# Performance work log

Measured on AMD Instinct MI355X. Metric: run time of the kernel, lower is better.

Reference implementation:

```python
import jax, jax.numpy as jnp
import numpy as np

B, S, D, H, R = 4, 4096, 1024, 16, 256
DEPTH = D // H  # 64
FILTER_H = 3


def setup_inputs() -> dict:
    key = jax.random.key(0)
    ks = jax.random.split(key, 10)
    s = 0.02
    return {
        "x": jax.random.normal(ks[0], (B, S, D), jnp.float32),
        "wq": jax.random.normal(ks[1], (D, D), jnp.float32) * s,
        "wk": jax.random.normal(ks[2], (D, D), jnp.float32) * s,
        "wv": jax.random.normal(ks[3], (D, D), jnp.float32) * s,
        "E": jax.random.normal(ks[4], (H, S, R), jnp.float32) * s,
        "F": jax.random.normal(ks[5], (H, S, R), jnp.float32) * s,
        "conv_kernel": jax.random.normal(ks[6], (FILTER_H, R, 1, 1), jnp.float32) * s,  # HWIO
        "conv_bias": jnp.zeros((1,), jnp.float32),
        "wo": jax.random.normal(ks[7], (D, D), jnp.float32) * s,
        "bo": jnp.zeros((D,), jnp.float32),
    }


def _split_heads(t):
    # [B,S,D] -> [B,H,S,depth]
    return t.reshape(B, S, H, DEPTH).transpose(0, 2, 1, 3)


def reference(x, wq, wk, wv, E, F, conv_kernel, conv_bias, wo, bo):
    q = _split_heads(x @ wq)
    k = _split_heads(x @ wk)
    v = _split_heads(x @ wv)
    # low-rank projections along sequence: [B,H,R,depth]
    k_proj = jnp.einsum('bhnd,hnr->bhrd', k, E)
    v_proj = jnp.einsum('bhnd,hnr->bhrd', v, F)
    scale = 1.0 / jnp.sqrt(jnp.asarray(DEPTH, jnp.float32))
    scores = jnp.einsum('bhsd,bhrd->bhsr', q, k_proj) * scale  # [B,H,S,R]
    # Conv2D(filters=1, kernel=(3,R), padding='same') over [B*H, S, R, 1]
    xi = scores.reshape(B * H, S, R, 1)
    conv = jax.lax.conv_general_dilated(
        xi, conv_kernel, window_strides=(1, 1), padding='SAME',
        dimension_numbers=('NHWC', 'HWIO', 'NHWC'))
    scores = (conv + conv_bias).reshape(B, H, S, R)
    attn = jax.nn.softmax(scores, axis=-1)
    out = jnp.einsum('bhsr,bhrd->bhsd', attn, v_proj)
    out = out.transpose(0, 2, 1, 3).reshape(B, S, D)
    return out @ wo + bo
```

## Files before the change

### kernel.cpp

```cpp
#include <hip/hip_runtime.h>

#define B_ 4
#define S_ 4096
#define D_ 1024
#define H_ 16
#define R_ 256
#define DP_ 64

typedef short bf16x8 __attribute__((ext_vector_type(8)));
typedef short short4v __attribute__((ext_vector_type(4)));
typedef float f32x4 __attribute__((ext_vector_type(4)));

__device__ __forceinline__ short f2bf(float f) {
  unsigned u = __builtin_bit_cast(unsigned, f);
  u += 0x7fffu + ((u >> 16) & 1u);
  return (short)(u >> 16);
}
__device__ __forceinline__ float bf2f(short s) {
  unsigned u = ((unsigned)(unsigned short)s) << 16;
  return __builtin_bit_cast(float, u);
}

__global__ __launch_bounds__(256) void convert_x_kernel(const float* __restrict__ x,
                                                        short* __restrict__ xb) {
  const int n8 = (B_ * S_ * D_) / 8;
  int i = blockIdx.x * 256 + threadIdx.x;
  const int stride = gridDim.x * 256;
  for (; i < n8; i += stride) {
    const float4 a = ((const float4*)x)[2 * i];
    const float4 b = ((const float4*)x)[2 * i + 1];
    bf16x8 o;
    o[0] = f2bf(a.x); o[1] = f2bf(a.y); o[2] = f2bf(a.z); o[3] = f2bf(a.w);
    o[4] = f2bf(b.x); o[5] = f2bf(b.y); o[6] = f2bf(b.z); o[7] = f2bf(b.w);
    ((bf16x8*)xb)[i] = o;
  }
}

__global__ __launch_bounds__(256) void transpose_w_kernel(
    const float* __restrict__ w0, const float* __restrict__ w1,
    const float* __restrict__ w2, const float* __restrict__ w3,
    short* __restrict__ wT) {
  __shared__ float tile[64][65];
  const int z = blockIdx.z;
  const float* W = (z == 0) ? w0 : (z == 1) ? w1 : (z == 2) ? w2 : w3;
  short* out = wT + (size_t)z * (D_ * D_);
  const int k0 = blockIdx.y * 64;
  const int n0 = blockIdx.x * 64;
  const int tid = threadIdx.x;
#pragma unroll
  for (int q = 0; q < 4; ++q) {
    const int rr = (tid >> 4) + (q << 4);
    const float4 v = *(const float4*)&W[(size_t)(k0 + rr) * D_ + n0 + ((tid & 15) << 2)];
    tile[rr][(tid & 15) * 4 + 0] = v.x;
    tile[rr][(tid & 15) * 4 + 1] = v.y;
    tile[rr][(tid & 15) * 4 + 2] = v.z;
    tile[rr][(tid & 15) * 4 + 3] = v.w;
  }
  __syncthreads();
#pragma unroll
  for (int q = 0; q < 2; ++q) {
    const int nr = (tid >> 3) + (q << 5);
    const int c8 = (tid & 7) << 3;
    bf16x8 o;
#pragma unroll
    for (int j = 0; j < 8; ++j) o[j] = f2bf(tile[c8 + j][nr]);
    *(bf16x8*)&out[(size_t)(n0 + nr) * D_ + k0 + c8] = o;
  }
}

__global__ __launch_bounds__(256) void build_T_kernel(const float* __restrict__ ck,
                                                      short* __restrict__ Tt) {
  const int idx = blockIdx.x * 256 + threadIdx.x;
  const int i = idx >> 16;
  const int r = (idx >> 8) & 255;
  const int c = idx & 255;
  const int j = c - r + 127;
  const float v = (j >= 0 && j < 256) ? ck[i * 256 + j] * 0.125f : 0.f;
  Tt[idx] = f2bf(v);
}

template <bool OUT_BF16>
__device__ __forceinline__ void mfma_gemm_1024(const short* __restrict__ A,
                                               const short* __restrict__ Bt,
                                               void* __restrict__ Cout,
                                               const float* __restrict__ bias) {
  __shared__ short As[128 * 32];
  __shared__ short Bs[128 * 32];
  const int tid = threadIdx.x;
  const int w = tid >> 6, l = tid & 63;
  const int m0 = blockIdx.y * 128, n0 = blockIdx.x * 128;

  const int srow = (w << 5) + (l >> 2);
  const int gchunk = l & 3;
  const int schunkX = ((gchunk ^ (srow & 3)) << 4);
  const short* Ag = A + (size_t)(m0 + srow) * D_ + (gchunk << 3);
  const short* Bg = Bt + (size_t)(n0 + srow) * D_ + (gchunk << 3);
  char* AsW = (char*)As + srow * 64 + schunkX;
  char* BsW = (char*)Bs + srow * 64 + schunkX;

  const int wr = ((w >> 1) << 6);
  const int wc = ((w & 1) << 6);
  const int fx = (l >> 4) ^ (l & 3);

  f32x4 acc[4][4];
#pragma unroll
  for (int i = 0; i < 4; ++i)
#pragma unroll
    for (int j = 0; j < 4; ++j) acc[i][j] = (f32x4){0.f, 0.f, 0.f, 0.f};

  for (int k0 = 0; k0 < D_; k0 += 32) {
    const bf16x8 a0 = *(const bf16x8*)(Ag + k0);
    const bf16x8 a1 = *(const bf16x8*)(Ag + (size_t)16 * D_ + k0);
    const bf16x8 b0 = *(const bf16x8*)(Bg + k0);
    const bf16x8 b1 = *(const bf16x8*)(Bg + (size_t)16 * D_ + k0);
    __syncthreads();
    *(bf16x8*)AsW = a0;
    *(bf16x8*)(AsW + 1024) = a1;
    *(bf16x8*)BsW = b0;
    *(bf16x8*)(BsW + 1024) = b1;
    __syncthreads();
    bf16x8 af[4], bfv[4];
#pragma unroll
    for (int t = 0; t < 4; ++t) {
      const int ar = wr + (t << 4) + (l & 15);
      af[t] = *(const bf16x8*)((char*)As + ar * 64 + (fx << 4));
      const int br = wc + (t << 4) + (l & 15);
      bfv[t] = *(const bf16x8*)((char*)Bs + br * 64 + (fx << 4));
    }
#pragma unroll
    for (int i = 0; i < 4; ++i)
#pragma unroll
      for (int j = 0; j < 4; ++j)
        acc[i][j] = __builtin_amdgcn_mfma_f32_16x16x32_bf16(af[i], bfv[j], acc[i][j], 0, 0, 0);
  }

#pragma unroll
  for (int i = 0; i < 4; ++i) {
#pragma unroll
    for (int r = 0; r < 4; ++r) {
      const int row = m0 + wr + (i << 4) + ((l >> 4) << 2) + r;
#pragma unroll
      for (int j = 0; j < 4; ++j) {
        const int col = n0 + wc + (j << 4) + (l & 15);
        const float vv = acc[i][j][r];
        if (OUT_BF16)
          ((short*)Cout)[(size_t)row * D_ + col] = f2bf(vv);
        else
          ((float*)Cout)[(size_t)row * D_ + col] = vv + bias[col];
      }
    }
  }
}

__global__ __launch_bounds__(256) void qkv_mfma_kernel(
    const short* __restrict__ xb, const short* __restrict__ wT,
    short* __restrict__ qb, short* __restrict__ kb, short* __restrict__ vb) {
  const int z = blockIdx.z;
  const short* Bt = wT + (size_t)z * (D_ * D_);
  short* C = (z == 0) ? qb : (z == 1) ? kb : vb;
  mfma_gemm_1024<true>(xb, Bt, C, nullptr);
}

__global__ __launch_bounds__(256) void out_mfma_kernel(
    const short* __restrict__ aob, const short* __restrict__ woT,
    const float* __restrict__ bo, float* __restrict__ out) {
  mfma_gemm_1024<false>(aob, woT, out, bo);
}

__global__ __launch_bounds__(256) void transpose_kv_kernel(
    const short* __restrict__ kb, const short* __restrict__ vb,
    short* __restrict__ kTb, short* __restrict__ vTb) {
  __shared__ short tile[64 * 80];
  const int tid = threadIdx.x;
  const int n0 = blockIdx.x * 64;
  const int bh = blockIdx.y;
  const int b = bh >> 4, h = bh & 15;
  const short* src = blockIdx.z ? vb : kb;
  short* dst = blockIdx.z ? vTb : kTb;
#pragma unroll
  for (int q = 0; q < 2; ++q) {
    const int idx = tid + q * 256;
    const int n = idx >> 3, c = idx & 7;
    *(bf16x8*)&tile[n * 80 + c * 8] =
        *(const bf16x8*)&src[((size_t)b * S_ + n0 + n) * D_ + h * DP_ + c * 8];
  }
  __syncthreads();
#pragma unroll
  for (int q = 0; q < 2; ++q) {
    const int idx = tid + q * 256;
    const int d = idx >> 3, cc = idx & 7;
    bf16x8 o;
#pragma unroll
    for (int j = 0; j < 8; ++j) o[j] = tile[(cc * 8 + j) * 80 + d];
    *(bf16x8*)&dst[((size_t)bh * DP_ + d) * S_ + n0 + cc * 8] = o;
  }
}

__global__ __launch_bounds__(256) void transpose_EF_kernel(
    const float* __restrict__ E, const float* __restrict__ F,
    short* __restrict__ ETb, short* __restrict__ FTb) {
  __shared__ float tile[64][65];
  const int tid = threadIdx.x;
  const int n0 = blockIdx.x * 64;
  const int r0 = blockIdx.y * 64;
  const int hz = blockIdx.z;
  const int h = hz & 15;
  const float* src = (hz < 16) ? E : F;
  short* dst = (hz < 16) ? ETb : FTb;
  const float* base = src + ((size_t)h * S_ + n0) * R_ + r0;
#pragma unroll
  for (int q = 0; q < 4; ++q) {
    const int n = (tid >> 4) + q * 16;
    const int r4 = (tid & 15) << 2;
    const float4 v = *(const float4*)&base[(size_t)n * R_ + r4];
    tile[n][r4 + 0] = v.x; tile[n][r4 + 1] = v.y;
    tile[n][r4 + 2] = v.z; tile[n][r4 + 3] = v.w;
  }
  __syncthreads();
#pragma unroll
  for (int q = 0; q < 2; ++q) {
    const int r = (tid >> 3) + q * 32;
    const int n8 = (tid & 7) << 3;
    bf16x8 o;
#pragma unroll
    for (int j = 0; j < 8; ++j) o[j] = f2bf(tile[n8 + j][r]);
    *(bf16x8*)&dst[((size_t)h * R_ + r0 + r) * S_ + n0 + n8] = o;
  }
}

__global__ __launch_bounds__(256) void proj_mfma_kernel(
    const short* __restrict__ ETb, const short* __restrict__ FTb,
    const short* __restrict__ kTb, const short* __restrict__ vTb,
    short* __restrict__ kprojTb, short* __restrict__ vprojTb) {
  __shared__ short As[128 * 64];
  __shared__ short Bs[64 * 64];
  const int tid = threadIdx.x;
  const int w = tid >> 6, l = tid & 63;
  const int l15 = l & 15, l16 = l >> 4;
  const int r0 = blockIdx.x * 128;
  const int bh = blockIdx.y;
  const int h = bh & 15;
  const int z = blockIdx.z;
  const short* Ab = (z ? FTb : ETb) + ((size_t)h * R_ + r0) * S_;
  const short* Bb = (z ? vTb : kTb) + (size_t)bh * DP_ * S_;
  short* outp = z ? vprojTb : kprojTb;
  const int wm = w >> 1, wn = w & 1;

  f32x4 acc[4][2];
#pragma unroll
  for (int mt = 0; mt < 4; ++mt)
#pragma unroll
    for (int nt = 0; nt < 2; ++nt) acc[mt][nt] = (f32x4){0.f, 0.f, 0.f, 0.f};

  for (int k0 = 0; k0 < S_; k0 += 64) {
    bf16x8 a[4], bq[2];
#pragma unroll
    for (int j = 0; j < 4; ++j) {
      const int idx = tid + j * 256;
      const int ar = idx >> 3, c = idx & 7;
      a[j] = *(const bf16x8*)&Ab[(size_t)ar * S_ + k0 + c * 8];
    }
#pragma unroll
    for (int j = 0; j < 2; ++j) {
      const int idx = tid + j * 256;
      const int br = idx >> 3, c = idx & 7;
      bq[j] = *(const bf16x8*)&Bb[(size_t)br * S_ + k0 + c * 8];
    }
    __syncthreads();
#pragma unroll
    for (int j = 0; j < 4; ++j) {
      const int idx = tid + j * 256;
      const int ar = idx >> 3, c = idx & 7;
      *(bf16x8*)((char*)As + ar * 128 + ((c ^ (ar & 7)) << 4)) = a[j];
    }
#pragma unroll
    for (int j = 0; j < 2; ++j) {
      const int idx = tid + j * 256;
      const int br = idx >> 3, c = idx & 7;
      *(bf16x8*)((char*)Bs + br * 128 + ((c ^ (br & 7)) << 4)) = bq[j];
    }
    __syncthreads();
#pragma unroll
    for (int kk = 0; kk < 2; ++kk) {
      bf16x8 af[4], bfr[2];
#pragma unroll
      for (int mt = 0; mt < 4; ++mt) {
        const int row = wm * 64 + mt * 16 + l15;
        af[mt] = *(const bf16x8*)((char*)As + row * 128 + (((kk * 4 + l16) ^ (row & 7)) << 4));
      }
#pragma unroll
      for (int nt = 0; nt < 2; ++nt) {
        const int row = wn * 32 + nt * 16 + l15;
        bfr[nt] = *(const bf16x8*)((char*)Bs + row * 128 + (((kk * 4 + l16) ^ (row & 7)) << 4));
      }
#pragma unroll
      for (int mt = 0; mt < 4; ++mt)
#pragma unroll
        for (int nt = 0; nt < 2; ++nt)
          acc[mt][nt] = __builtin_amdgcn_mfma_f32_16x16x32_bf16(af[mt], bfr[nt], acc[mt][nt], 0, 0, 0);
    }
  }

#pragma unroll
  for (int mt = 0; mt < 4; ++mt)
#pragma unroll
    for (int nt = 0; nt < 2; ++nt) {
      const int d = wn * 32 + nt * 16 + l15;
      const int rbase = r0 + wm * 64 + mt * 16 + l16 * 4;
      short4v o;
#pragma unroll
      for (int rr = 0; rr < 4; ++rr) o[rr] = f2bf(acc[mt][nt][rr]);
      *(short4v*)&outp[((size_t)bh * DP_ + d) * R_ + rbase] = o;
    }
}

__global__ __launch_bounds__(256) void build_M_kernel(
    const short* __restrict__ Tt, const short* __restrict__ kprojTb,
    short* __restrict__ Mb) {
  const int tid = threadIdx.x;
  const int w = tid >> 6, l = tid & 63;
  const int l15 = l & 15, l16 = l >> 4;
  const int r0 = blockIdx.x * 64 + w * 16;
  const int bh = blockIdx.y;
  const short* Kp = kprojTb + (size_t)bh * DP_ * R_;

#pragma unroll
  for (int i = 0; i < 3; ++i) {
    const short* Ti = Tt + (size_t)i * (R_ * R_);
    f32x4 acc[4];
#pragma unroll
    for (int n = 0; n < 4; ++n) acc[n] = (f32x4){0.f, 0.f, 0.f, 0.f};
#pragma unroll
    for (int kk = 0; kk < 8; ++kk) {
      const bf16x8 av = *(const bf16x8*)&Ti[(size_t)(r0 + l15) * R_ + kk * 32 + l16 * 8];
#pragma unroll
      for (int n = 0; n < 4; ++n) {
        const bf16x8 bv = *(const bf16x8*)&Kp[(size_t)(n * 16 + l15) * R_ + kk * 32 + l16 * 8];
        acc[n] = __builtin_amdgcn_mfma_f32_16x16x32_bf16(av, bv, acc[n], 0, 0, 0);
      }
    }
    short* Mo = Mb + (((size_t)bh * 3 + i) * R_) * DP_;
#pragma unroll
    for (int n = 0; n < 4; ++n)
#pragma unroll
      for (int rr = 0; rr < 4; ++rr)
        Mo[(size_t)(r0 + l16 * 4 + rr) * DP_ + n * 16 + l15] = f2bf(acc[n][rr]);
  }
}

__global__ __launch_bounds__(256) void attn_fused_kernel(
    const short* __restrict__ qb, const short* __restrict__ Mb,
    const short* __restrict__ vprojTb, short* __restrict__ aob) {
  __shared__ char smem[32768 + 66 * 144];
  const int tid = threadIdx.x;
  const int w = tid >> 6, l = tid & 63;
  const int l15 = l & 15, l16 = l >> 4;
  const int s0 = blockIdx.x * 64;
  const int bh = blockIdx.y;
  const int b = bh >> 4, h = bh & 15;

  for (int idx = tid; idx < 66 * 8; idx += 256) {
    const int t = idx >> 3, c = idx & 7;
    const int s = s0 - 1 + t;
    bf16x8 val = {0, 0, 0, 0, 0, 0, 0, 0};
    if (s >= 0 && s < S_)
      val = *(const bf16x8*)&qb[((size_t)(b * S_ + s)) * D_ + h * DP_ + c * 8];
    *(bf16x8*)(smem + 32768 + t * 144 + c * 16) = val;
  }
  __syncthreads();

  f32x4 acc[4][4];
#pragma unroll
  for (int m = 0; m < 4; ++m)
#pragma unroll
    for (int n = 0; n < 4; ++n) acc[m][n] = (f32x4){0.f, 0.f, 0.f, 0.f};

  const short* Mbh = Mb + (size_t)bh * 3 * R_ * DP_;
#pragma unroll
  for (int i = 0; i < 3; ++i) {
    bf16x8 qf[4][2];
#pragma unroll
    for (int m = 0; m < 4; ++m)
#pragma unroll
      for (int kk = 0; kk < 2; ++kk)
        qf[m][kk] = *(const bf16x8*)(smem + 32768 + (m * 16 + l15 + i) * 144 +
                                     ((kk * 4 + l16) << 4));
    const short* Mi = Mbh + (size_t)i * R_ * DP_;
#pragma unroll
    for (int n = 0; n < 4; ++n) {
      const short* mrow = Mi + (size_t)(w * 64 + n * 16 + l15) * DP_ + l16 * 8;
      const bf16x8 m0 = *(const bf16x8*)mrow;
      const bf16x8 m1 = *(const bf16x8*)(mrow + 32);
#pragma unroll
      for (int m = 0; m < 4; ++m) {
        acc[m][n] = __builtin_amdgcn_mfma_f32_16x16x32_bf16(qf[m][0], m0, acc[m][n], 0, 0, 0);
        acc[m][n] = __builtin_amdgcn_mfma_f32_16x16x32_bf16(qf[m][1], m1, acc[m][n], 0, 0, 0);
      }
    }
  }
#pragma unroll
  for (int m = 0; m < 4; ++m)
#pragma unroll
    for (int n = 0; n < 4; ++n)
#pragma unroll
      for (int rr = 0; rr < 4; ++rr) {
        const int t = m * 16 + l16 * 4 + rr;
        const int c = w * 64 + n * 16 + l15;
        const int off = t * 512 + (((c >> 3) ^ (t & 7)) << 4) + ((c & 7) << 1);
        *(short*)(smem + off) = f2bf(acc[m][n][rr]);
      }
  __syncthreads();

  {
    const int g = l >> 4, u = l & 15;
#pragma unroll
    for (int it = 0; it < 4; ++it) {
      const int t = w * 16 + it * 4 + g;
      const int off0 = t * 512 + (((u * 2) ^ (t & 7)) << 4);
      const int off1 = t * 512 + (((u * 2 + 1) ^ (t & 7)) << 4);
      bf16x8 p0 = *(bf16x8*)(smem + off0);
      bf16x8 p1 = *(bf16x8*)(smem + off1);
      float f[16];
#pragma unroll
      for (int j = 0; j < 8; ++j) { f[j] = bf2f(p0[j]); f[8 + j] = bf2f(p1[j]); }
      float mx = f[0];
#pragma unroll
      for (int j = 1; j < 16; ++j) mx = fmaxf(mx, f[j]);
#pragma unroll
      for (int d = 1; d < 16; d <<= 1) mx = fmaxf(mx, __shfl_xor(mx, d, 64));
      float sm = 0.f;
#pragma unroll
      for (int j = 0; j < 16; ++j) { f[j] = __expf(f[j] - mx); sm += f[j]; }
#pragma unroll
      for (int d = 1; d < 16; d <<= 1) sm += __shfl_xor(sm, d, 64);
      const float inv = 1.f / sm;
#pragma unroll
      for (int j = 0; j < 8; ++j) { p0[j] = f2bf(f[j] * inv); p1[j] = f2bf(f[8 + j] * inv); }
      *(bf16x8*)(smem + off0) = p0;
      *(bf16x8*)(smem + off1) = p1;
    }
  }
  __syncthreads();

  f32x4 pacc[4];
#pragma unroll
  for (int n = 0; n < 4; ++n) pacc[n] = (f32x4){0.f, 0.f, 0.f, 0.f};
#pragma unroll
  for (int kk = 0; kk < 8; ++kk) {
    const int row = w * 16 + l15;
    const int ck = kk * 4 + l16;
    const bf16x8 pa = *(const bf16x8*)(smem + row * 512 + ((ck ^ (row & 7)) << 4));
#pragma unroll
    for (int n = 0; n < 4; ++n) {
      const bf16x8 bv = *(const bf16x8*)(vprojTb + ((size_t)bh * DP_ + n * 16 + l15) * R_ +
                                         (kk << 5) + (l16 << 3));
      pacc[n] = __builtin_amdgcn_mfma_f32_16x16x32_bf16(pa, bv, pacc[n], 0, 0, 0);
    }
  }
#pragma unroll
  for (int n = 0; n < 4; ++n)
#pragma unroll
    for (int rr = 0; rr < 4; ++rr) {
      const int s = s0 + w * 16 + l16 * 4 + rr;
      const int d = n * 16 + l15;
      aob[((size_t)(b * S_ + s)) * D_ + h * DP_ + d] = f2bf(pacc[n][rr]);
    }
}

extern "C" void kernel_launch(void* const* d_in, const int* in_sizes, int n_in,
                              void* d_out, int out_size, void* d_ws, size_t ws_size,
                              hipStream_t stream) {
  const float* x = (const float*)d_in[0];
  const float* wq = (const float*)d_in[1];
  const float* wk = (const float*)d_in[2];
  const float* wv = (const float*)d_in[3];
  const float* E = (const float*)d_in[4];
  const float* F = (const float*)d_in[5];
  const float* ck = (const float*)d_in[6];
  const float* wo = (const float*)d_in[8];
  const float* bo = (const float*)d_in[9];
  float* out = (float*)d_out;

  const size_t QN = (size_t)B_ * S_ * D_;
  const size_t WN = (size_t)D_ * D_;
  const size_t TN = (size_t)DP_ * S_ * 64;
  const size_t PN = (size_t)64 * R_ * DP_;

  short* xb = (short*)d_ws;
  short* wT = xb + QN;
  short* qb = wT + 4 * WN;
  short* kb = qb + QN;
  short* vb = kb + QN;
  short* kTb = vb + QN;
  short* vTb = kTb + TN;
  short* kprojTb = vTb + TN;
  short* vprojTb = kprojTb + PN;
  short* Tt = vprojTb + PN;
  short* ETb = xb;
  short* FTb = kb;
  short* Mb = xb;
  short* aob = vb;

  convert_x_kernel<<<2048, 256, 0, stream>>>(x, xb);
  {
    dim3 g(16, 16, 4);
    transpose_w_kernel<<<g, 256, 0, stream>>>(wq, wk, wv, wo, wT);
  }
  {
    dim3 g(D_ / 128, (B_ * S_) / 128, 3);
    qkv_mfma_kernel<<<g, 256, 0, stream>>>(xb, wT, qb, kb, vb);
  }
  build_T_kernel<<<768, 256, 0, stream>>>(ck, Tt);
  {
    dim3 g(S_ / 64, B_ * H_, 2);
    transpose_kv_kernel<<<g, 256, 0, stream>>>(kb, vb, kTb, vTb);
  }
  {
    dim3 g(S_ / 64, R_ / 64, 32);
    transpose_EF_kernel<<<g, 256, 0, stream>>>(E, F, ETb, FTb);
  }
  {
    dim3 g(2, 64, 2);
    proj_mfma_kernel<<<g, 256, 0, stream>>>(ETb, FTb, kTb, vTb, kprojTb, vprojTb);
  }
  {
    dim3 g(4, 64);
    build_M_kernel<<<g, 256, 0, stream>>>(Tt, kprojTb, Mb);
  }
  {
    dim3 g(S_ / 64, B_ * H_);
    attn_fused_kernel<<<g, 256, 0, stream>>>(qb, Mb, vprojTb, aob);
  }
  {
    dim3 g(D_ / 128, (B_ * S_) / 128);
    out_mfma_kernel<<<g, 256, 0, stream>>>(aob, wT + 3 * WN, bo, out);
  }
}
```

Before: 693.8 us.

## Fuse K/V transpose into QKV GEMM epilogue and use direct global-to-LDS loads

```diff
diff --git a/kernel.cpp b/kernel.cpp
--- a/kernel.cpp
+++ b/kernel.cpp
@@ -10,6 +10,7 @@
 typedef short bf16x8 __attribute__((ext_vector_type(8)));
 typedef short short4v __attribute__((ext_vector_type(4)));
 typedef float f32x4 __attribute__((ext_vector_type(4)));
+typedef unsigned int u32;
 
 __device__ __forceinline__ short f2bf(float f) {
   unsigned u = __builtin_bit_cast(unsigned, f);
@@ -19,6 +20,11 @@
 __device__ __forceinline__ float bf2f(short s) {
   unsigned u = ((unsigned)(unsigned short)s) << 16;
   return __builtin_bit_cast(float, u);
+}
+
+__device__ __forceinline__ void gload16(const short* g, short* l) {
+  __builtin_amdgcn_global_load_lds((const __attribute__((address_space(1))) u32*)g,
+                                   (__attribute__((address_space(3))) u32*)l, 16, 0, 0);
 }
 
 __global__ __launch_bounds__(256) void convert_x_kernel(const float* __restrict__ x,
@@ -79,121 +85,123 @@
   Tt[idx] = f2bf(v);
 }
 
-template <bool OUT_BF16>
-__device__ __forceinline__ void mfma_gemm_1024(const short* __restrict__ A,
+__device__ __forceinline__ void gemm_core_1024(const short* __restrict__ A,
                                                const short* __restrict__ Bt,
-                                               void* __restrict__ Cout,
-                                               const float* __restrict__ bias) {
+                                               int m0, int n0, f32x4 acc[4][4]) {
   __shared__ short As[128 * 32];
   __shared__ short Bs[128 * 32];
   const int tid = threadIdx.x;
   const int w = tid >> 6, l = tid & 63;
-  const int m0 = blockIdx.y * 128, n0 = blockIdx.x * 128;
-
-  const int srow = (w << 5) + (l >> 2);
-  const int gchunk = l & 3;
-  const int schunkX = ((gchunk ^ (srow & 3)) << 4);
-  const short* Ag = A + (size_t)(m0 + srow) * D_ + (gchunk << 3);
-  const short* Bg = Bt + (size_t)(n0 + srow) * D_ + (gchunk << 3);
-  char* AsW = (char*)As + srow * 64 + schunkX;
-  char* BsW = (char*)Bs + srow * 64 + schunkX;
-
-  const int wr = ((w >> 1) << 6);
-  const int wc = ((w & 1) << 6);
-  const int fx = (l >> 4) ^ (l & 3);
-
-  f32x4 acc[4][4];
-#pragma unroll
-  for (int i = 0; i < 4; ++i)
-#pragma unroll
-    for (int j = 0; j < 4; ++j) acc[i][j] = (f32x4){0.f, 0.f, 0.f, 0.f};
+  const int l15 = l & 15, l16 = l >> 4;
+  const int wr = (w >> 1) << 6, wc = (w & 1) << 6;
+
+  const short* Ag = A + (size_t)(m0 + w * 32 + (l >> 2)) * D_ + (l & 3) * 8;
+  const short* Bg = Bt + (size_t)(n0 + w * 32 + (l >> 2)) * D_ + (l & 3) * 8;
+  short* AsD = As + w * 1024;
+  short* BsD = Bs + w * 1024;
 
   for (int k0 = 0; k0 < D_; k0 += 32) {
-    const bf16x8 a0 = *(const bf16x8*)(Ag + k0);
-    const bf16x8 a1 = *(const bf16x8*)(Ag + (size_t)16 * D_ + k0);
-    const bf16x8 b0 = *(const bf16x8*)(Bg + k0);
-    const bf16x8 b1 = *(const bf16x8*)(Bg + (size_t)16 * D_ + k0);
     __syncthreads();
-    *(bf16x8*)AsW = a0;
-    *(bf16x8*)(AsW + 1024) = a1;
-    *(bf16x8*)BsW = b0;
-    *(bf16x8*)(BsW + 1024) = b1;
+    gload16(Ag + k0, AsD);
+    gload16(Ag + k0 + 16 * D_, AsD + 512);
+    gload16(Bg + k0, BsD);
+    gload16(Bg + k0 + 16 * D_, BsD + 512);
     __syncthreads();
-    bf16x8 af[4], bfv[4];
+    bf16x8 af[4], bv[4];
 #pragma unroll
     for (int t = 0; t < 4; ++t) {
-      const int ar = wr + (t << 4) + (l & 15);
-      af[t] = *(const bf16x8*)((char*)As + ar * 64 + (fx << 4));
-      const int br = wc + (t << 4) + (l & 15);
-      bfv[t] = *(const bf16x8*)((char*)Bs + br * 64 + (fx << 4));
+      af[t] = *(const bf16x8*)(As + (wr + t * 16 + l15) * 32 + l16 * 8);
+      bv[t] = *(const bf16x8*)(Bs + (wc + t * 16 + l15) * 32 + l16 * 8);
     }
 #pragma unroll
     for (int i = 0; i < 4; ++i)
 #pragma unroll
       for (int j = 0; j < 4; ++j)
-        acc[i][j] = __builtin_amdgcn_mfma_f32_16x16x32_bf16(af[i], bfv[j], acc[i][j], 0, 0, 0);
-  }
-
-#pragma unroll
-  for (int i = 0; i < 4; ++i) {
-#pragma unroll
-    for (int r = 0; r < 4; ++r) {
-      const int row = m0 + wr + (i << 4) + ((l >> 4) << 2) + r;
-#pragma unroll
-      for (int j = 0; j < 4; ++j) {
-        const int col = n0 + wc + (j << 4) + (l & 15);
-        const float vv = acc[i][j][r];
-        if (OUT_BF16)
-          ((short*)Cout)[(size_t)row * D_ + col] = f2bf(vv);
-        else
-          ((float*)Cout)[(size_t)row * D_ + col] = vv + bias[col];
-      }
-    }
+        acc[i][j] = __builtin_amdgcn_mfma_f32_16x16x32_bf16(af[i], bv[j], acc[i][j], 0, 0, 0);
   }
 }
 
 __global__ __launch_bounds__(256) void qkv_mfma_kernel(
     const short* __restrict__ xb, const short* __restrict__ wT,
-    short* __restrict__ qb, short* __restrict__ kb, short* __restrict__ vb) {
-  const int z = blockIdx.z;
-  const short* Bt = wT + (size_t)z * (D_ * D_);
-  short* C = (z == 0) ? qb : (z == 1) ? kb : vb;
-  mfma_gemm_1024<true>(xb, Bt, C, nullptr);
+    short* __restrict__ qb, short* __restrict__ kTb, short* __restrict__ vTb) {
+  const int wg = blockIdx.x;
+  const int swz = (wg & 7) * 384 + (wg >> 3);
+  const int nx = swz % 24, my = swz / 24;
+  const int m0 = my * 128, n0 = nx * 128;
+
+  f32x4 acc[4][4];
+#pragma unroll
+  for (int i = 0; i < 4; ++i)
+#pragma unroll
+    for (int j = 0; j < 4; ++j) acc[i][j] = (f32x4){0.f, 0.f, 0.f, 0.f};
+  gemm_core_1024(xb, wT, m0, n0, acc);
+
+  const int tid = threadIdx.x;
+  const int w = tid >> 6, l = tid & 63;
+  const int l15 = l & 15, l16 = l >> 4;
+  const int wr = (w >> 1) << 6, wc = (w & 1) << 6;
+
+  if (n0 < 1024) {
+#pragma unroll
+    for (int i = 0; i < 4; ++i)
+#pragma unroll
+      for (int j = 0; j < 4; ++j)
+#pragma unroll
+        for (int rr = 0; rr < 4; ++rr) {
+          const int row = m0 + wr + i * 16 + l16 * 4 + rr;
+          const int col = n0 + wc + j * 16 + l15;
+          qb[(size_t)row * D_ + col] = f2bf(acc[i][j][rr]);
+        }
+  } else {
+    short* dst = (n0 < 2048) ? kTb : vTb;
+    const int cb = n0 - ((n0 < 2048) ? 1024 : 2048);
+#pragma unroll
+    for (int i = 0; i < 4; ++i)
+#pragma unroll
+      for (int j = 0; j < 4; ++j) {
+        const int col = cb + wc + j * 16 + l15;
+        const int h = col >> 6, d = col & 63;
+        const int rowb = m0 + wr + i * 16 + l16 * 4;
+        const int b = rowb >> 12, nseq = rowb & 4095;
+        short4v o;
+#pragma unroll
+        for (int rr = 0; rr < 4; ++rr) o[rr] = f2bf(acc[i][j][rr]);
+        *(short4v*)&dst[(((size_t)(b * 16 + h) * 64 + d) << 12) + nseq] = o;
+      }
+  }
 }
 
 __global__ __launch_bounds__(256) void out_mfma_kernel(
     const short* __restrict__ aob, const short* __restrict__ woT,
     const float* __restrict__ bo, float* __restrict__ out) {
-  mfma_gemm_1024<false>(aob, woT, out, bo);
-}
-
-__global__ __launch_bounds__(256) void transpose_kv_kernel(
-    const short* __restrict__ kb, const short* __restrict__ vb,
-    short* __restrict__ kTb, short* __restrict__ vTb) {
-  __shared__ short tile[64 * 80];
-  const int tid = threadIdx.x;
-  const int n0 = blockIdx.x * 64;
-  const int bh = blockIdx.y;
-  const int b = bh >> 4, h = bh & 15;
-  const short* src = blockIdx.z ? vb : kb;
-  short* dst = blockIdx.z ? vTb : kTb;
-#pragma unroll
-  for (int q = 0; q < 2; ++q) {
-    const int idx = tid + q * 256;
-    const int n = idx >> 3, c = idx & 7;
-    *(bf16x8*)&tile[n * 80 + c * 8] =
-        *(const bf16x8*)&src[((size_t)b * S_ + n0 + n) * D_ + h * DP_ + c * 8];
-  }
-  __syncthreads();
-#pragma unroll
-  for (int q = 0; q < 2; ++q) {
-    const int idx = tid + q * 256;
-    const int d = idx >> 3, cc = idx & 7;
-    bf16x8 o;
-#pragma unroll
-    for (int j = 0; j < 8; ++j) o[j] = tile[(cc * 8 + j) * 80 + d];
-    *(bf16x8*)&dst[((size_t)bh * DP_ + d) * S_ + n0 + cc * 8] = o;
-  }
+  const int wg = blockIdx.x;
+  const int swz = (wg & 7) * 128 + (wg >> 3);
+  const int nx = swz & 7, my = swz >> 3;
+  const int m0 = my * 128, n0 = nx * 128;
+
+  f32x4 acc[4][4];
+#pragma unroll
+  for (int i = 0; i < 4; ++i)
+#pragma unroll
+    for (int j = 0; j < 4; ++j) acc[i][j] = (f32x4){0.f, 0.f, 0.f, 0.f};
+  gemm_core_1024(aob, woT, m0, n0, acc);
+
+  const int tid = threadIdx.x;
+  const int w = tid >> 6, l = tid & 63;
+  const int l15 = l & 15, l16 = l >> 4;
+  const int wr = (w >> 1) << 6, wc = (w & 1) << 6;
+#pragma unroll
+  for (int i = 0; i < 4; ++i)
+#pragma unroll
+    for (int j = 0; j < 4; ++j) {
+      const int col = n0 + wc + j * 16 + l15;
+      const float bb = bo[col];
+#pragma unroll
+      for (int rr = 0; rr < 4; ++rr) {
+        const int row = m0 + wr + i * 16 + l16 * 4 + rr;
+        out[(size_t)row * D_ + col] = acc[i][j][rr] + bb;
+      }
+    }
 }
 
 __global__ __launch_bounds__(256) void transpose_EF_kernel(
@@ -238,8 +246,9 @@
   const int w = tid >> 6, l = tid & 63;
   const int l15 = l & 15, l16 = l >> 4;
   const int r0 = blockIdx.x * 128;
-  const int bh = blockIdx.y;
-  const int h = bh & 15;
+  const int y = blockIdx.y;
+  const int h = y >> 2, b = y & 3;
+  const int bh = b * 16 + h;
   const int z = blockIdx.z;
   const short* Ab = (z ? FTb : ETb) + ((size_t)h * R_ + r0) * S_;
   const short* Bb = (z ? vTb : kTb) + (size_t)bh * DP_ * S_;
@@ -483,38 +492,28 @@
 
   const size_t QN = (size_t)B_ * S_ * D_;
   const size_t WN = (size_t)D_ * D_;
-  const size_t TN = (size_t)DP_ * S_ * 64;
   const size_t PN = (size_t)64 * R_ * DP_;
 
   short* xb = (short*)d_ws;
   short* wT = xb + QN;
   short* qb = wT + 4 * WN;
-  short* kb = qb + QN;
-  short* vb = kb + QN;
-  short* kTb = vb + QN;
-  short* vTb = kTb + TN;
-  short* kprojTb = vTb + TN;
+  short* kTb = qb + QN;
+  short* vTb = kTb + QN;
+  short* FTb = vTb + QN;
+  short* kprojTb = FTb + QN;
   short* vprojTb = kprojTb + PN;
   short* Tt = vprojTb + PN;
   short* ETb = xb;
-  short* FTb = kb;
   short* Mb = xb;
-  short* aob = vb;
+  short* aob = vTb;
 
   convert_x_kernel<<<2048, 256, 0, stream>>>(x, xb);
   {
     dim3 g(16, 16, 4);
     transpose_w_kernel<<<g, 256, 0, stream>>>(wq, wk, wv, wo, wT);
   }
-  {
-    dim3 g(D_ / 128, (B_ * S_) / 128, 3);
-    qkv_mfma_kernel<<<g, 256, 0, stream>>>(xb, wT, qb, kb, vb);
-  }
+  qkv_mfma_kernel<<<3072, 256, 0, stream>>>(xb, wT, qb, kTb, vTb);
   build_T_kernel<<<768, 256, 0, stream>>>(ck, Tt);
-  {
-    dim3 g(S_ / 64, B_ * H_, 2);
-    transpose_kv_kernel<<<g, 256, 0, stream>>>(kb, vb, kTb, vTb);
-  }
   {
     dim3 g(S_ / 64, R_ / 64, 32);
     transpose_EF_kernel<<<g, 256, 0, stream>>>(E, F, ETb, FTb);
@@ -531,8 +530,5 @@
     dim3 g(S_ / 64, B_ * H_);
     attn_fused_kernel<<<g, 256, 0, stream>>>(qb, Mb, vprojTb, aob);
   }
-  {
-    dim3 g(D_ / 128, (B_ * S_) / 128);
-    out_mfma_kernel<<<g, 256, 0, stream>>>(aob, wT + 3 * WN, bo, out);
-  }
-}
+  out_mfma_kernel<<<1024, 256, 0, stream>>>(aob, wT + 3 * WN, bo, out);
+}
```

Result: faster. 657.1 us (-5.3%).
